# Optimization experiments

Measured on AMD Instinct MI355X. Metric: run time of the kernel, lower is better.

## Reference

```python
import jax, jax.numpy as jnp
import numpy as np

B, T, F, H, P = 256, 512, 64, 512, 24  # batch, seq_len, fea_dim, hidden, pred_sequence


def setup_inputs() -> dict:
    key = jax.random.key(0)
    ks = jax.random.split(key, 7)
    s = 1.0 / np.sqrt(H)  # PyTorch default init scale
    u = lambda k, shp: jax.random.uniform(k, shp, jnp.float32, -s, s)
    return {
        "x": jax.random.normal(ks[0], (B, T, F), jnp.float32),
        "W_ih": u(ks[1], (4 * H, F)),
        "W_hh": u(ks[2], (4 * H, H)),
        "b_ih": u(ks[3], (4 * H,)),
        "b_hh": u(ks[4], (4 * H,)),
        "W_fc": u(ks[5], (P * F, H)),
        "b_fc": u(ks[6], (P * F,)),
    }


def reference(x, W_ih, W_hh, b_ih, b_hh, W_fc, b_fc):
    b, t, f = x.shape
    h4 = W_hh.shape[1]
    # Precompute input contribution to gates for all timesteps: [B,T,4H]
    x_gates = jnp.einsum('btf,gf->btg', x, W_ih) + b_ih + b_hh

    def step(carry, xg):  # xg: [B,4H]
        h, c = carry
        gates = xg + h @ W_hh.T  # [B,4H]
        i, fg, g, o = jnp.split(gates, 4, axis=-1)  # PyTorch gate order i,f,g,o
        i = jax.nn.sigmoid(i)
        fg = jax.nn.sigmoid(fg)
        o = jax.nn.sigmoid(o)
        g = jnp.tanh(g)
        c = fg * c + i * g
        h = o * jnp.tanh(c)
        return (h, c), None

    h0 = jnp.zeros((b, h4), x.dtype)
    c0 = jnp.zeros((b, h4), x.dtype)
    (hn, cn), _ = jax.lax.scan(step, (h0, c0), jnp.swapaxes(x_gates, 0, 1))
    # hn.squeeze() for num_layers=1 -> [B,H]; fc head then reshape to [B,P,F]
    out = hn @ W_fc.T + b_fc
    return out.reshape(-1, P, f)
```

## Files before the change

kernel.cpp:

```cpp
#include <hip/hip_runtime.h>
#include <stdint.h>


namespace {
constexpr int T_STEPS = 512;
constexpr int FEA  = 64;
constexpr int HID  = 512;
constexpr int KTOT = HID + FEA;
constexpr int KPAD = KTOT + 8;
constexpr int NKI  = KTOT / 32;
constexpr int GSTR = 132;
constexpr int RPG  = 16;
constexpr size_t DPAR     = 256ull * 256;
constexpr size_t FLAG_OFF = 2 * DPAR;
constexpr size_t GRZ_OFF  = FLAG_OFF + 16 * 16;

typedef __bf16   bf16x8 __attribute__((ext_vector_type(8)));
typedef uint16_t u16x8  __attribute__((ext_vector_type(8)));
typedef float    f32x4  __attribute__((ext_vector_type(4)));
typedef uint32_t u32x4  __attribute__((ext_vector_type(4)));

union V8 { u16x8 u; bf16x8 b; u32x4 q; };

__device__ __forceinline__ float bf2f(uint16_t u) {
  union { uint32_t i; float f; } v; v.i = (uint32_t)u << 16; return v.f;
}
__device__ __forceinline__ uint16_t f2bf(float f) {
  union { float f; uint32_t i; } v; v.f = f;
  uint32_t x = v.i;
  return (uint16_t)((x + 0x7FFFu + ((x >> 16) & 1u)) >> 16);
}
__device__ __forceinline__ float sigmoid_f(float x) {
  return 1.0f / (1.0f + __expf(-x));
}
__device__ __forceinline__ float tanh_f(float x) {
  float e = __expf(-2.0f * fabsf(x));
  float t = (1.0f - e) / (1.0f + e);
  return copysignf(t, x);
}
__device__ __forceinline__ bf16x8 load8(const void* base, size_t elem_off,
                                        bool fp32m) {
  V8 r;
  if (fp32m) {
    const float* p = (const float*)base + elem_off;
#pragma unroll
    for (int i = 0; i < 8; ++i) r.u[i] = f2bf(p[i]);
  } else {
    r.q = *(const u32x4*)((const uint16_t*)base + elem_off);
  }
  return r.b;
}
__device__ __forceinline__ float loadf(const void* base, int idx, bool fp32m) {
  return fp32m ? ((const float*)base)[idx] : bf2f(((const uint16_t*)base)[idx]);
}

__device__ __forceinline__ uint32_t ld32_sc01(const uint32_t* p) {
  uint32_t v;
  asm volatile("global_load_dword %0, %1, off sc0 sc1"
               : "=v"(v) : "v"(p) : "memory");
  return v;
}
__device__ __forceinline__ u32x4 ld128_sc01(const uint32_t* p) {
  u32x4 v;
  asm volatile("global_load_dwordx4 %0, %1, off sc0 sc1"
               : "=v"(v) : "v"(p) : "memory");
  return v;
}
__device__ __forceinline__ void st32_x(uint32_t* p, uint32_t v, bool xl) {
  if (xl) asm volatile("global_store_dword %0, %1, off sc0"
                       :: "v"(p), "v"(v) : "memory");
  else    asm volatile("global_store_dword %0, %1, off sc0 sc1"
                       :: "v"(p), "v"(v) : "memory");
}
__device__ __forceinline__ void waitcnt_vm0() {
  asm volatile("s_waitcnt vmcnt(0)" ::: "memory");
}
}

__global__ __launch_bounds__(256, 1) void lstm_persistent(
    const void* __restrict__ x,
    const void* __restrict__ W_ih,
    const void* __restrict__ W_hh,
    const void* __restrict__ b_ih,
    const void* __restrict__ b_hh,
    const void* __restrict__ W_fc,
    const void* __restrict__ b_fc,
    void* __restrict__ out,
    uint32_t* __restrict__ dbuf)
{
  __shared__ uint16_t Als[RPG * KPAD];
  __shared__ float    Gls[RPG * GSTR];
  __shared__ int      sflag, sok;

  const int tid = threadIdx.x;
  const int wv  = tid >> 6;
  const int ln  = tid & 63;
  const int nl  = ln & 15;
  const int kq  = ln >> 4;
  const int bg  = blockIdx.x & 15;
  const int wgi = blockIdx.x >> 4;
  const int r0  = bg * RPG;

  if (tid == 0) {
    uint32_t xcc;
    asm volatile("s_getreg_b32 %0, hwreg(HW_REG_XCC_ID)" : "=s"(xcc));
    unsigned* gmask = (unsigned*)(dbuf + GRZ_OFF) + bg;
    unsigned* gcnt  = (unsigned*)(dbuf + GRZ_OFF) + 16 + bg;
    atomicOr(gmask, 1u << (xcc & 31));
    __threadfence();
    atomicAdd(gcnt, 1u);
    while (atomicAdd(gcnt, 0u) < 16u) __builtin_amdgcn_s_sleep(1);
    __threadfence();
    unsigned m = atomicOr(gmask, 0u);
    sok = (__popc(m) == 1) ? 1 : 0;
  }

  if (tid == 1) sflag = 0;
  __syncthreads();
  {
    float a = fabsf(bf2f(((const uint16_t*)b_ih)[tid]));
    if (a > 1.0f) atomicOr(&sflag, 1);
  }
  __syncthreads();
  const bool fp32m = (sflag != 0);
  const bool xloc  = (sok != 0);

  bf16x8 breg[2][NKI];
  float  bias[2];
#pragma unroll
  for (int s = 0; s < 2; ++s) {
    int col  = wv * 32 + s * 16 + nl;
    int gate = col & 3;
    int unit = col >> 2;
    int gcol = gate * HID + wgi * 32 + unit;
#pragma unroll
    for (int kk = 0; kk < NKI; ++kk) {
      int k0 = kk * 32 + kq * 8;
      if (k0 < HID)
        breg[s][kk] = load8(W_hh, (size_t)gcol * HID + k0, fp32m);
      else
        breg[s][kk] = load8(W_ih, (size_t)gcol * FEA + (k0 - HID), fp32m);
    }
    bias[s] = loadf(b_ih, gcol, fp32m) + loadf(b_hh, gcol, fp32m);
  }

  const int ar  = tid >> 4;
  const int au  = (tid & 15) * 2;
  const int hdw = (r0 + ar) * 256 + wgi * 16 + (tid & 15);
  float c0 = 0.0f, c1 = 0.0f;

  const int srow = tid >> 4;
  const int l16  = tid & 15;
  uint16_t* Ar = &Als[srow * KPAD];

  uint32_t* flags = dbuf + FLAG_OFF + bg * 16;

  {
    u32x4 z = {0, 0, 0, 0};
#pragma unroll
    for (int i = 0; i < 4; ++i) *(u32x4*)&Ar[(l16 + 16 * i) * 8] = z;
    int xo = l16 * 4;
    size_t off = (size_t)(r0 + srow) * (T_STEPS * FEA) + xo;
    uint2 w;
    if (fp32m) {
      const float4 xv = *(const float4*)((const float*)x + off);
      w.x = (uint32_t)f2bf(xv.x) | ((uint32_t)f2bf(xv.y) << 16);
      w.y = (uint32_t)f2bf(xv.z) | ((uint32_t)f2bf(xv.w) << 16);
    } else {
      w = *(const uint2*)((const uint16_t*)x + off);
    }
    *(uint2*)&Ar[HID + xo] = w;
  }

  for (int t = 0; t < T_STEPS; ++t) {
    __syncthreads();

    f32x4 acc0, acc1;
    acc0[0] = bias[0]; acc0[1] = bias[0]; acc0[2] = bias[0]; acc0[3] = bias[0];
    acc1[0] = bias[1]; acc1[1] = bias[1]; acc1[2] = bias[1]; acc1[3] = bias[1];
#pragma unroll
    for (int kk = 0; kk < NKI; ++kk) {
      bf16x8 a = *(const bf16x8*)&Als[nl * KPAD + kk * 32 + kq * 8];
      acc0 = __builtin_amdgcn_mfma_f32_16x16x32_bf16(a, breg[0][kk], acc0, 0, 0, 0);
      acc1 = __builtin_amdgcn_mfma_f32_16x16x32_bf16(a, breg[1][kk], acc1, 0, 0, 0);
    }
#pragma unroll
    for (int r = 0; r < 4; ++r) {
      Gls[(kq * 4 + r) * GSTR + wv * 32 + nl]      = acc0[r];
      Gls[(kq * 4 + r) * GSTR + wv * 32 + 16 + nl] = acc1[r];
    }
    __syncthreads();

    {
      const f32x4* gp = (const f32x4*)&Gls[ar * GSTR + au * 4];
      f32x4 ga = gp[0], gb = gp[1];
      c0 = sigmoid_f(ga[1]) * c0 + sigmoid_f(ga[0]) * tanh_f(ga[2]);
      float h0 = sigmoid_f(ga[3]) * tanh_f(c0);
      c1 = sigmoid_f(gb[1]) * c1 + sigmoid_f(gb[0]) * tanh_f(gb[2]);
      float h1 = sigmoid_f(gb[3]) * tanh_f(c1);
      uint32_t hp = (uint32_t)f2bf(h0) | ((uint32_t)f2bf(h1) << 16);
      uint32_t* hw = dbuf + (size_t)((t + 1) & 1) * DPAR;
      st32_x(hw + hdw, hp, xloc);
    }
    waitcnt_vm0();
    __syncthreads();

    if (tid == 0) st32_x(flags + wgi, (uint32_t)(t + 1), xloc);
    if (t + 1 < T_STEPS) {
      int xo = l16 * 4;
      size_t off = (size_t)(r0 + srow) * (T_STEPS * FEA)
                   + (size_t)(t + 1) * FEA + xo;
      uint2 w;
      if (fp32m) {
        const float4 xv = *(const float4*)((const float*)x + off);
        w.x = (uint32_t)f2bf(xv.x) | ((uint32_t)f2bf(xv.y) << 16);
        w.y = (uint32_t)f2bf(xv.z) | ((uint32_t)f2bf(xv.w) << 16);
      } else {
        w = *(const uint2*)((const uint16_t*)x + off);
      }
      *(uint2*)&Ar[HID + xo] = w;
    }
    if (tid < 16) {
      const uint32_t* fp = flags + tid;
      uint32_t target = (uint32_t)(t + 1);
      for (;;) {
        uint32_t c = ld32_sc01(fp);
        waitcnt_vm0();
        if (c >= target) break;
      }
    }
    __syncthreads();

    if (t + 1 < T_STEPS) {
      const uint32_t* src = dbuf + (size_t)((t + 1) & 1) * DPAR
                          + (size_t)(r0 + srow) * 256;
      u32x4 v0 = ld128_sc01(src + (l16 + 0)  * 4);
      u32x4 v1 = ld128_sc01(src + (l16 + 16) * 4);
      u32x4 v2 = ld128_sc01(src + (l16 + 32) * 4);
      u32x4 v3 = ld128_sc01(src + (l16 + 48) * 4);
      waitcnt_vm0();
      *(u32x4*)&Ar[(l16 + 0)  * 8] = v0;
      *(u32x4*)&Ar[(l16 + 16) * 8] = v1;
      *(u32x4*)&Ar[(l16 + 32) * 8] = v2;
      *(u32x4*)&Ar[(l16 + 48) * 8] = v3;
    }
  }

  const uint32_t* hn = dbuf;
  int gwave = wgi * 4 + wv;
  for (int tile = gwave; tile < 96; tile += 64) {
    int n = tile * 16 + nl;
    float bs = loadf(b_fc, n, fp32m);
    f32x4 acc; acc[0] = bs; acc[1] = bs; acc[2] = bs; acc[3] = bs;
#pragma unroll
    for (int kk = 0; kk < 16; ++kk) {
      int k0 = kk * 32 + kq * 8;
      V8 av;
      av.q = ld128_sc01(hn + (size_t)(r0 + nl) * 256 + (k0 >> 1));
      bf16x8 b = load8(W_fc, (size_t)n * HID + k0, fp32m);
      waitcnt_vm0();
      acc = __builtin_amdgcn_mfma_f32_16x16x32_bf16(av.b, b, acc, 0, 0, 0);
    }
#pragma unroll
    for (int r = 0; r < 4; ++r) {
      int row = r0 + kq * 4 + r;
      if (fp32m) ((float*)out)[(size_t)row * 1536 + n] = acc[r];
      else       ((uint16_t*)out)[(size_t)row * 1536 + n] = f2bf(acc[r]);
    }
  }
}

extern "C" void kernel_launch(void* const* d_in, const int* in_sizes, int n_in,
                              void* d_out, int out_size, void* d_ws, size_t ws_size,
                              hipStream_t stream) {
  const void* x    = d_in[0];
  const void* W_ih = d_in[1];
  const void* W_hh = d_in[2];
  const void* b_ih = d_in[3];
  const void* b_hh = d_in[4];
  const void* W_fc = d_in[5];
  const void* b_fc = d_in[6];
  uint32_t* dbuf = (uint32_t*)d_ws;

  hipMemsetAsync((void*)(dbuf + FLAG_OFF), 0,
                 (16 * 16 + 32) * sizeof(uint32_t), stream);

  lstm_persistent<<<dim3(256), dim3(256), 0, stream>>>(
      x, W_ih, W_hh, b_ih, b_hh, W_fc, b_fc, d_out, dbuf);
}
```

Before: 1.042 ms.

## Replace block-level flag barrier with per-wave flags and direct global h loads

Restructures the per-timestep synchronisation of the persistent LSTM kernel. Each wave now publishes its own progress flag, and every wave polls all 16 producer flags in its batch group. Waves then load h straight from global memory into registers as MFMA A-operands, so the LDS staging buffer and two block-wide barriers per step are gone. The x-projection MFMAs are issued while the h loads are in flight, accumulation is split into two chains, and the gate buffer is double-buffered. The cost is more flag polling traffic per wave and heavier register use for the 16 prefetched h vectors.

```diff
diff --git a/kernel.cpp b/kernel.cpp
--- a/kernel.cpp
+++ b/kernel.cpp
@@ -6,14 +6,12 @@
 constexpr int T_STEPS = 512;
 constexpr int FEA  = 64;
 constexpr int HID  = 512;
-constexpr int KTOT = HID + FEA;
-constexpr int KPAD = KTOT + 8;
-constexpr int NKI  = KTOT / 32;
+constexpr int NKI  = 18;
 constexpr int GSTR = 132;
 constexpr int RPG  = 16;
-constexpr size_t DPAR     = 256ull * 256;
-constexpr size_t FLAG_OFF = 2 * DPAR;
-constexpr size_t GRZ_OFF  = FLAG_OFF + 16 * 16;
+constexpr size_t HBUF_DW = 256ull * 256;
+constexpr size_t FLAG_OFF = 2 * HBUF_DW;
+constexpr size_t GRZ_OFF  = FLAG_OFF + 16 * 64;
 
 typedef __bf16   bf16x8 __attribute__((ext_vector_type(8)));
 typedef uint16_t u16x8  __attribute__((ext_vector_type(8)));
@@ -71,6 +69,10 @@
                        :: "v"(p), "v"(v) : "memory");
   else    asm volatile("global_store_dword %0, %1, off sc0 sc1"
                        :: "v"(p), "v"(v) : "memory");
+}
+__device__ __forceinline__ void waitcnt_vm0_fence() {
+  asm volatile("s_waitcnt vmcnt(0)" ::: "memory");
+  __builtin_amdgcn_sched_barrier(0);
 }
 __device__ __forceinline__ void waitcnt_vm0() {
   asm volatile("s_waitcnt vmcnt(0)" ::: "memory");
@@ -88,9 +90,8 @@
     void* __restrict__ out,
     uint32_t* __restrict__ dbuf)
 {
-  __shared__ uint16_t Als[RPG * KPAD];
-  __shared__ float    Gls[RPG * GSTR];
-  __shared__ int      sflag, sok;
+  __shared__ float Gls[2][RPG * GSTR];
+  __shared__ int   sflag, sok;
 
   const int tid = threadIdx.x;
   const int wv  = tid >> 6;
@@ -149,117 +150,129 @@
   const int hdw = (r0 + ar) * 256 + wgi * 16 + (tid & 15);
   float c0 = 0.0f, c1 = 0.0f;
 
-  const int srow = tid >> 4;
-  const int l16  = tid & 15;
-  uint16_t* Ar = &Als[srow * KPAD];
-
-  uint32_t* flags = dbuf + FLAG_OFF + bg * 16;
-
-  {
-    u32x4 z = {0, 0, 0, 0};
-#pragma unroll
-    for (int i = 0; i < 4; ++i) *(u32x4*)&Ar[(l16 + 16 * i) * 8] = z;
-    int xo = l16 * 4;
-    size_t off = (size_t)(r0 + srow) * (T_STEPS * FEA) + xo;
-    uint2 w;
-    if (fp32m) {
-      const float4 xv = *(const float4*)((const float*)x + off);
-      w.x = (uint32_t)f2bf(xv.x) | ((uint32_t)f2bf(xv.y) << 16);
-      w.y = (uint32_t)f2bf(xv.z) | ((uint32_t)f2bf(xv.w) << 16);
-    } else {
-      w = *(const uint2*)((const uint16_t*)x + off);
-    }
-    *(uint2*)&Ar[HID + xo] = w;
-  }
+  uint32_t* flagw = dbuf + FLAG_OFF + bg * 64 + wgi * 4 + wv;
+  const uint32_t* fb = dbuf + FLAG_OFF + bg * 64 + (nl >> 2);
+
+  st32_x(dbuf + hdw, 0u, xloc);
+  waitcnt_vm0();
+  if (ln == 0) st32_x(flagw, 1u, xloc);
 
   for (int t = 0; t < T_STEPS; ++t) {
+    bf16x8 ax0, ax1;
+    {
+      size_t off = (size_t)(r0 + nl) * (T_STEPS * FEA) + (size_t)t * FEA
+                 + kq * 8;
+      if (fp32m) {
+        const float* xp = (const float*)x + off;
+        V8 a0v, a1v;
+#pragma unroll
+        for (int i = 0; i < 8; ++i) {
+          a0v.u[i] = f2bf(xp[i]); a1v.u[i] = f2bf(xp[32 + i]);
+        }
+        ax0 = a0v.b; ax1 = a1v.b;
+      } else {
+        const uint16_t* xp = (const uint16_t*)x + off;
+        ax0 = *(const bf16x8*)xp;
+        ax1 = *(const bf16x8*)(xp + 32);
+      }
+    }
+
+    {
+      const uint32_t tgt = (uint32_t)(t + 1);
+      uint32_t need = 0xFFFFu;
+      uint32_t fv[16];
+      for (;;) {
+#pragma unroll
+        for (int p = 0; p < 16; ++p)
+          if (need & (1u << p)) fv[p] = ld32_sc01(fb + p * 4);
+        waitcnt_vm0_fence();
+#pragma unroll
+        for (int p = 0; p < 16; ++p)
+          if ((need & (1u << p)) && fv[p] >= tgt) need &= ~(1u << p);
+        if (!need) break;
+      }
+    }
+
+    const uint32_t* hb = dbuf + (size_t)(t & 1) * HBUF_DW
+                       + (size_t)(r0 + nl) * 256 + kq * 4;
+    V8 av[16];
+#pragma unroll
+    for (int p = 0; p < 16; ++p) av[p].q = ld128_sc01(hb + p * 16);
+
+    f32x4 c0a, c0b, c1a, c1b;
+#pragma unroll
+    for (int i = 0; i < 4; ++i) {
+      c0a[i] = bias[0]; c1a[i] = bias[1]; c0b[i] = 0.0f; c1b[i] = 0.0f;
+    }
+    c0a = __builtin_amdgcn_mfma_f32_16x16x32_bf16(ax0, breg[0][16], c0a, 0, 0, 0);
+    c1a = __builtin_amdgcn_mfma_f32_16x16x32_bf16(ax0, breg[1][16], c1a, 0, 0, 0);
+    c0b = __builtin_amdgcn_mfma_f32_16x16x32_bf16(ax1, breg[0][17], c0b, 0, 0, 0);
+    c1b = __builtin_amdgcn_mfma_f32_16x16x32_bf16(ax1, breg[1][17], c1b, 0, 0, 0);
+    waitcnt_vm0_fence();
+
+#pragma unroll
+    for (int kk = 0; kk < 16; ++kk) {
+      if (kk & 1) {
+        c0b = __builtin_amdgcn_mfma_f32_16x16x32_bf16(av[kk].b, breg[0][kk], c0b, 0, 0, 0);
+        c1b = __builtin_amdgcn_mfma_f32_16x16x32_bf16(av[kk].b, breg[1][kk], c1b, 0, 0, 0);
+      } else {
+        c0a = __builtin_amdgcn_mfma_f32_16x16x32_bf16(av[kk].b, breg[0][kk], c0a, 0, 0, 0);
+        c1a = __builtin_amdgcn_mfma_f32_16x16x32_bf16(av[kk].b, breg[1][kk], c1a, 0, 0, 0);
+      }
+    }
+    f32x4 A0 = c0a + c0b, A1 = c1a + c1b;
+
+    float* G = Gls[t & 1];
+#pragma unroll
+    for (int r = 0; r < 4; ++r) {
+      G[(kq * 4 + r) * GSTR + wv * 32 + nl]      = A0[r];
+      G[(kq * 4 + r) * GSTR + wv * 32 + 16 + nl] = A1[r];
+    }
     __syncthreads();
 
-    f32x4 acc0, acc1;
-    acc0[0] = bias[0]; acc0[1] = bias[0]; acc0[2] = bias[0]; acc0[3] = bias[0];
-    acc1[0] = bias[1]; acc1[1] = bias[1]; acc1[2] = bias[1]; acc1[3] = bias[1];
-#pragma unroll
-    for (int kk = 0; kk < NKI; ++kk) {
-      bf16x8 a = *(const bf16x8*)&Als[nl * KPAD + kk * 32 + kq * 8];
-      acc0 = __builtin_amdgcn_mfma_f32_16x16x32_bf16(a, breg[0][kk], acc0, 0, 0, 0);
-      acc1 = __builtin_amdgcn_mfma_f32_16x16x32_bf16(a, breg[1][kk], acc1, 0, 0, 0);
-    }
-#pragma unroll
-    for (int r = 0; r < 4; ++r) {
-      Gls[(kq * 4 + r) * GSTR + wv * 32 + nl]      = acc0[r];
-      Gls[(kq * 4 + r) * GSTR + wv * 32 + 16 + nl] = acc1[r];
-    }
-    __syncthreads();
-
     {
-      const f32x4* gp = (const f32x4*)&Gls[ar * GSTR + au * 4];
+      const f32x4* gp = (const f32x4*)&Gls[t & 1][ar * GSTR + au * 4];
       f32x4 ga = gp[0], gb = gp[1];
       c0 = sigmoid_f(ga[1]) * c0 + sigmoid_f(ga[0]) * tanh_f(ga[2]);
       float h0 = sigmoid_f(ga[3]) * tanh_f(c0);
       c1 = sigmoid_f(gb[1]) * c1 + sigmoid_f(gb[0]) * tanh_f(gb[2]);
       float h1 = sigmoid_f(gb[3]) * tanh_f(c1);
       uint32_t hp = (uint32_t)f2bf(h0) | ((uint32_t)f2bf(h1) << 16);
-      uint32_t* hw = dbuf + (size_t)((t + 1) & 1) * DPAR;
-      st32_x(hw + hdw, hp, xloc);
-    }
-    waitcnt_vm0();
-    __syncthreads();
-
-    if (tid == 0) st32_x(flags + wgi, (uint32_t)(t + 1), xloc);
-    if (t + 1 < T_STEPS) {
-      int xo = l16 * 4;
-      size_t off = (size_t)(r0 + srow) * (T_STEPS * FEA)
-                   + (size_t)(t + 1) * FEA + xo;
-      uint2 w;
-      if (fp32m) {
-        const float4 xv = *(const float4*)((const float*)x + off);
-        w.x = (uint32_t)f2bf(xv.x) | ((uint32_t)f2bf(xv.y) << 16);
-        w.y = (uint32_t)f2bf(xv.z) | ((uint32_t)f2bf(xv.w) << 16);
-      } else {
-        w = *(const uint2*)((const uint16_t*)x + off);
-      }
-      *(uint2*)&Ar[HID + xo] = w;
-    }
-    if (tid < 16) {
-      const uint32_t* fp = flags + tid;
-      uint32_t target = (uint32_t)(t + 1);
-      for (;;) {
-        uint32_t c = ld32_sc01(fp);
-        waitcnt_vm0();
-        if (c >= target) break;
-      }
-    }
-    __syncthreads();
-
-    if (t + 1 < T_STEPS) {
-      const uint32_t* src = dbuf + (size_t)((t + 1) & 1) * DPAR
-                          + (size_t)(r0 + srow) * 256;
-      u32x4 v0 = ld128_sc01(src + (l16 + 0)  * 4);
-      u32x4 v1 = ld128_sc01(src + (l16 + 16) * 4);
-      u32x4 v2 = ld128_sc01(src + (l16 + 32) * 4);
-      u32x4 v3 = ld128_sc01(src + (l16 + 48) * 4);
+      st32_x(dbuf + (size_t)((t + 1) & 1) * HBUF_DW + hdw, hp, xloc);
       waitcnt_vm0();
-      *(u32x4*)&Ar[(l16 + 0)  * 8] = v0;
-      *(u32x4*)&Ar[(l16 + 16) * 8] = v1;
-      *(u32x4*)&Ar[(l16 + 32) * 8] = v2;
-      *(u32x4*)&Ar[(l16 + 48) * 8] = v3;
-    }
-  }
-
-  const uint32_t* hn = dbuf;
+      if (ln == 0) st32_x(flagw, (uint32_t)(t + 2), xloc);
+    }
+  }
+
+  {
+    const uint32_t tgt = (uint32_t)(T_STEPS + 1);
+    uint32_t need = 0xFFFFu;
+    uint32_t fv[16];
+    for (;;) {
+#pragma unroll
+      for (int p = 0; p < 16; ++p)
+        if (need & (1u << p)) fv[p] = ld32_sc01(fb + p * 4);
+      waitcnt_vm0_fence();
+#pragma unroll
+      for (int p = 0; p < 16; ++p)
+        if ((need & (1u << p)) && fv[p] >= tgt) need &= ~(1u << p);
+      if (!need) break;
+    }
+  }
   int gwave = wgi * 4 + wv;
   for (int tile = gwave; tile < 96; tile += 64) {
     int n = tile * 16 + nl;
     float bs = loadf(b_fc, n, fp32m);
     f32x4 acc; acc[0] = bs; acc[1] = bs; acc[2] = bs; acc[3] = bs;
+    const uint32_t* hb = dbuf + (size_t)(r0 + nl) * 256 + kq * 4;
+    V8 av[16];
+#pragma unroll
+    for (int p = 0; p < 16; ++p) av[p].q = ld128_sc01(hb + p * 16);
+    waitcnt_vm0_fence();
 #pragma unroll
     for (int kk = 0; kk < 16; ++kk) {
-      int k0 = kk * 32 + kq * 8;
-      V8 av;
-      av.q = ld128_sc01(hn + (size_t)(r0 + nl) * 256 + (k0 >> 1));
-      bf16x8 b = load8(W_fc, (size_t)n * HID + k0, fp32m);
-      waitcnt_vm0();
-      acc = __builtin_amdgcn_mfma_f32_16x16x32_bf16(av.b, b, acc, 0, 0, 0);
+      bf16x8 b = load8(W_fc, (size_t)n * HID + kk * 32 + kq * 8, fp32m);
+      acc = __builtin_amdgcn_mfma_f32_16x16x32_bf16(av[kk].b, b, acc, 0, 0, 0);
     }
 #pragma unroll
     for (int r = 0; r < 4; ++r) {
@@ -283,7 +296,7 @@
   uint32_t* dbuf = (uint32_t*)d_ws;
 
   hipMemsetAsync((void*)(dbuf + FLAG_OFF), 0,
-                 (16 * 16 + 32) * sizeof(uint32_t), stream);
+                 (16 * 64 + 32) * sizeof(uint32_t), stream);
 
   lstm_persistent<<<dim3(256), dim3(256), 0, stream>>>(
       x, W_ih, W_hh, b_ih, b_hh, W_fc, b_fc, d_out, dbuf);
```

New measurement: 2.182 ms. +109.4%, slower.

## Use per-wave completion flags and k-major LDS layout to cut per-step barriers

Applied to the files above, without the earlier changes.

Each wave now publishes its own step flag right after storing its hidden values, so the post-store workgroup barrier is gone. Pollers read four flags with one 128-bit load and take their minimum. The shared A tile is re-laid out k-major with a padded pitch to change the LDS bank pattern, and the FC head issues all its hidden-state loads before waiting. The cost is four times as many flags to poll, which adds memory traffic on the hot spin path.

```diff
diff --git a/kernel.cpp b/kernel.cpp
--- a/kernel.cpp
+++ b/kernel.cpp
@@ -6,14 +6,13 @@
 constexpr int T_STEPS = 512;
 constexpr int FEA  = 64;
 constexpr int HID  = 512;
-constexpr int KTOT = HID + FEA;
-constexpr int KPAD = KTOT + 8;
-constexpr int NKI  = KTOT / 32;
+constexpr int NKI  = 18;
 constexpr int GSTR = 132;
 constexpr int RPG  = 16;
-constexpr size_t DPAR     = 256ull * 256;
-constexpr size_t FLAG_OFF = 2 * DPAR;
-constexpr size_t GRZ_OFF  = FLAG_OFF + 16 * 16;
+constexpr int GPITCH = 136;
+constexpr size_t HBUF_DW  = 256ull * 256;
+constexpr size_t FLAG_OFF = 2 * HBUF_DW;
+constexpr size_t GRZ_OFF  = FLAG_OFF + 16 * 64;
 
 typedef __bf16   bf16x8 __attribute__((ext_vector_type(8)));
 typedef uint16_t u16x8  __attribute__((ext_vector_type(8)));
@@ -53,13 +52,18 @@
 __device__ __forceinline__ float loadf(const void* base, int idx, bool fp32m) {
   return fp32m ? ((const float*)base)[idx] : bf2f(((const uint16_t*)base)[idx]);
 }
-
-__device__ __forceinline__ uint32_t ld32_sc01(const uint32_t* p) {
-  uint32_t v;
-  asm volatile("global_load_dword %0, %1, off sc0 sc1"
-               : "=v"(v) : "v"(p) : "memory");
-  return v;
-}
+__device__ __forceinline__ uint2 ldx4(const void* x, size_t elem_off,
+                                      bool fp32m) {
+  if (fp32m) {
+    float4 v = *(const float4*)((const float*)x + elem_off);
+    uint2 w;
+    w.x = (uint32_t)f2bf(v.x) | ((uint32_t)f2bf(v.y) << 16);
+    w.y = (uint32_t)f2bf(v.z) | ((uint32_t)f2bf(v.w) << 16);
+    return w;
+  }
+  return *(const uint2*)((const uint16_t*)x + elem_off);
+}
+
 __device__ __forceinline__ u32x4 ld128_sc01(const uint32_t* p) {
   u32x4 v;
   asm volatile("global_load_dwordx4 %0, %1, off sc0 sc1"
@@ -74,6 +78,10 @@
 }
 __device__ __forceinline__ void waitcnt_vm0() {
   asm volatile("s_waitcnt vmcnt(0)" ::: "memory");
+}
+__device__ __forceinline__ void waitcnt_vm0_fence() {
+  asm volatile("s_waitcnt vmcnt(0)" ::: "memory");
+  __builtin_amdgcn_sched_barrier(0);
 }
 }
 
@@ -88,9 +96,9 @@
     void* __restrict__ out,
     uint32_t* __restrict__ dbuf)
 {
-  __shared__ uint16_t Als[RPG * KPAD];
-  __shared__ float    Gls[RPG * GSTR];
-  __shared__ int      sflag, sok;
+  __shared__ __align__(16) uint16_t Als[72 * GPITCH];
+  __shared__ float Gls[RPG * GSTR];
+  __shared__ int   sflag, sok;
 
   const int tid = threadIdx.x;
   const int wv  = tid >> 6;
@@ -150,26 +158,21 @@
   float c0 = 0.0f, c1 = 0.0f;
 
   const int srow = tid >> 4;
-  const int l16  = tid & 15;
-  uint16_t* Ar = &Als[srow * KPAD];
-
-  uint32_t* flags = dbuf + FLAG_OFF + bg * 16;
+  const int sc   = tid & 15;
+
+  uint32_t* flagw = dbuf + FLAG_OFF + bg * 64 + wgi * 4 + wv;
+  const uint32_t* fb0 = dbuf + FLAG_OFF + bg * 64;
 
   {
     u32x4 z = {0, 0, 0, 0};
-#pragma unroll
-    for (int i = 0; i < 4; ++i) *(u32x4*)&Ar[(l16 + 16 * i) * 8] = z;
-    int xo = l16 * 4;
-    size_t off = (size_t)(r0 + srow) * (T_STEPS * FEA) + xo;
-    uint2 w;
-    if (fp32m) {
-      const float4 xv = *(const float4*)((const float*)x + off);
-      w.x = (uint32_t)f2bf(xv.x) | ((uint32_t)f2bf(xv.y) << 16);
-      w.y = (uint32_t)f2bf(xv.z) | ((uint32_t)f2bf(xv.w) << 16);
-    } else {
-      w = *(const uint2*)((const uint16_t*)x + off);
-    }
-    *(uint2*)&Ar[HID + xo] = w;
+    for (int i = tid; i < 64 * GPITCH / 8; i += 256)
+      *(u32x4*)&Als[i * 8] = z;
+  }
+  {
+    int gx = sc & 7, hf = sc >> 3;
+    size_t off = (size_t)(r0 + srow) * (T_STEPS * FEA) + gx * 8 + hf * 4;
+    uint2 w = ldx4(x, off, fp32m);
+    *(uint2*)&Als[(64 + gx) * GPITCH + srow * 8 + hf * 4] = w;
   }
 
   for (int t = 0; t < T_STEPS; ++t) {
@@ -180,7 +183,7 @@
     acc1[0] = bias[1]; acc1[1] = bias[1]; acc1[2] = bias[1]; acc1[3] = bias[1];
 #pragma unroll
     for (int kk = 0; kk < NKI; ++kk) {
-      bf16x8 a = *(const bf16x8*)&Als[nl * KPAD + kk * 32 + kq * 8];
+      bf16x8 a = *(const bf16x8*)&Als[(4 * kk + kq) * GPITCH + nl * 8];
       acc0 = __builtin_amdgcn_mfma_f32_16x16x32_bf16(a, breg[0][kk], acc0, 0, 0, 0);
       acc1 = __builtin_amdgcn_mfma_f32_16x16x32_bf16(a, breg[1][kk], acc1, 0, 0, 0);
     }
@@ -190,6 +193,9 @@
       Gls[(kq * 4 + r) * GSTR + wv * 32 + 16 + nl] = acc1[r];
     }
     __syncthreads();
+
+    const uint32_t tg = (uint32_t)(t + 1);
+    const bool havex = (t + 1 < T_STEPS);
 
     {
       const f32x4* gp = (const f32x4*)&Gls[ar * GSTR + au * 4];
@@ -199,67 +205,62 @@
       c1 = sigmoid_f(gb[1]) * c1 + sigmoid_f(gb[0]) * tanh_f(gb[2]);
       float h1 = sigmoid_f(gb[3]) * tanh_f(c1);
       uint32_t hp = (uint32_t)f2bf(h0) | ((uint32_t)f2bf(h1) << 16);
-      uint32_t* hw = dbuf + (size_t)((t + 1) & 1) * DPAR;
-      st32_x(hw + hdw, hp, xloc);
-    }
-    waitcnt_vm0();
+      st32_x(dbuf + (size_t)(tg & 1) * HBUF_DW + hdw, hp, xloc);
+      waitcnt_vm0();
+      if (ln == 0) st32_x(flagw, tg, xloc);
+    }
+
+    if (havex) {
+      int gx = sc & 7, hf = sc >> 3;
+      size_t off = (size_t)(r0 + srow) * (T_STEPS * FEA)
+                 + (size_t)(t + 1) * FEA + gx * 8 + hf * 4;
+      uint2 w = ldx4(x, off, fp32m);
+      *(uint2*)&Als[(64 + gx) * GPITCH + srow * 8 + hf * 4] = w;
+    }
+
+    if (tid < 16) {
+      const uint32_t* fp = fb0 + tid * 4;
+      for (;;) {
+        u32x4 f = ld128_sc01(fp);
+        waitcnt_vm0_fence();
+        uint32_t mn = f[0];
+        mn = f[1] < mn ? f[1] : mn;
+        mn = f[2] < mn ? f[2] : mn;
+        mn = f[3] < mn ? f[3] : mn;
+        if (mn >= tg) break;
+      }
+    }
     __syncthreads();
 
-    if (tid == 0) st32_x(flags + wgi, (uint32_t)(t + 1), xloc);
-    if (t + 1 < T_STEPS) {
-      int xo = l16 * 4;
-      size_t off = (size_t)(r0 + srow) * (T_STEPS * FEA)
-                   + (size_t)(t + 1) * FEA + xo;
-      uint2 w;
-      if (fp32m) {
-        const float4 xv = *(const float4*)((const float*)x + off);
-        w.x = (uint32_t)f2bf(xv.x) | ((uint32_t)f2bf(xv.y) << 16);
-        w.y = (uint32_t)f2bf(xv.z) | ((uint32_t)f2bf(xv.w) << 16);
-      } else {
-        w = *(const uint2*)((const uint16_t*)x + off);
-      }
-      *(uint2*)&Ar[HID + xo] = w;
-    }
-    if (tid < 16) {
-      const uint32_t* fp = flags + tid;
-      uint32_t target = (uint32_t)(t + 1);
-      for (;;) {
-        uint32_t c = ld32_sc01(fp);
-        waitcnt_vm0();
-        if (c >= target) break;
-      }
-    }
-    __syncthreads();
-
-    if (t + 1 < T_STEPS) {
-      const uint32_t* src = dbuf + (size_t)((t + 1) & 1) * DPAR
+    if (havex) {
+      const uint32_t* src = dbuf + (size_t)(tg & 1) * HBUF_DW
                           + (size_t)(r0 + srow) * 256;
-      u32x4 v0 = ld128_sc01(src + (l16 + 0)  * 4);
-      u32x4 v1 = ld128_sc01(src + (l16 + 16) * 4);
-      u32x4 v2 = ld128_sc01(src + (l16 + 32) * 4);
-      u32x4 v3 = ld128_sc01(src + (l16 + 48) * 4);
+      u32x4 v0 = ld128_sc01(src + (sc + 0)  * 4);
+      u32x4 v1 = ld128_sc01(src + (sc + 16) * 4);
+      u32x4 v2 = ld128_sc01(src + (sc + 32) * 4);
+      u32x4 v3 = ld128_sc01(src + (sc + 48) * 4);
       waitcnt_vm0();
-      *(u32x4*)&Ar[(l16 + 0)  * 8] = v0;
-      *(u32x4*)&Ar[(l16 + 16) * 8] = v1;
-      *(u32x4*)&Ar[(l16 + 32) * 8] = v2;
-      *(u32x4*)&Ar[(l16 + 48) * 8] = v3;
-    }
-  }
-
-  const uint32_t* hn = dbuf;
+      *(u32x4*)&Als[(sc + 0)  * GPITCH + srow * 8] = v0;
+      *(u32x4*)&Als[(sc + 16) * GPITCH + srow * 8] = v1;
+      *(u32x4*)&Als[(sc + 32) * GPITCH + srow * 8] = v2;
+      *(u32x4*)&Als[(sc + 48) * GPITCH + srow * 8] = v3;
+    }
+  }
+
   int gwave = wgi * 4 + wv;
   for (int tile = gwave; tile < 96; tile += 64) {
     int n = tile * 16 + nl;
     float bs = loadf(b_fc, n, fp32m);
     f32x4 acc; acc[0] = bs; acc[1] = bs; acc[2] = bs; acc[3] = bs;
+    const uint32_t* hb = dbuf + (size_t)(r0 + nl) * 256 + kq * 4;
+    V8 av[16];
+#pragma unroll
+    for (int p = 0; p < 16; ++p) av[p].q = ld128_sc01(hb + p * 16);
+    waitcnt_vm0_fence();
 #pragma unroll
     for (int kk = 0; kk < 16; ++kk) {
-      int k0 = kk * 32 + kq * 8;
-      V8 av;
-      av.q = ld128_sc01(hn + (size_t)(r0 + nl) * 256 + (k0 >> 1));
-      bf16x8 b = load8(W_fc, (size_t)n * HID + k0, fp32m);
-      waitcnt_vm0();
-      acc = __builtin_amdgcn_mfma_f32_16x16x32_bf16(av.b, b, acc, 0, 0, 0);
+      bf16x8 b = load8(W_fc, (size_t)n * HID + kk * 32 + kq * 8, fp32m);
+      acc = __builtin_amdgcn_mfma_f32_16x16x32_bf16(av[kk].b, b, acc, 0, 0, 0);
     }
 #pragma unroll
     for (int r = 0; r < 4; ++r) {
@@ -283,7 +284,7 @@
   uint32_t* dbuf = (uint32_t*)d_ws;
 
   hipMemsetAsync((void*)(dbuf + FLAG_OFF), 0,
-                 (16 * 16 + 32) * sizeof(uint32_t), stream);
+                 (16 * 64 + 32) * sizeof(uint32_t), stream);
 
   lstm_persistent<<<dim3(256), dim3(256), 0, stream>>>(
       x, W_ih, W_hh, b_ih, b_hh, W_fc, b_fc, d_out, dbuf);
```

After: 1.033 ms. Within noise of the previous version (-0.8%).
